# Kernel tuning notes

Measured on AMD Instinct MI355X. Metric: run time of the kernel, lower is better.

The kernel has to match this reference:

```python
import jax, jax.numpy as jnp
import numpy as np

INF_MIN = -10000.0
B, S, VOCAB = 256, 1024, 126
T = VOCAB + 2           # tag_size
START, END = T - 2, T - 1


def setup_inputs() -> dict:
    key = jax.random.key(0)
    k1, k2, k3 = jax.random.split(key, 3)
    features = jax.random.normal(k1, (B, S, T), dtype=jnp.float32)
    batch_len = jax.random.randint(k2, (B,), 1, S + 1, dtype=jnp.int32)
    transitions = jax.random.normal(k3, (T, T), dtype=jnp.float32)
    # CRF structural constraints set at init: nothing transitions INTO start,
    # nothing transitions OUT of end.
    transitions = transitions.at[:, START].set(INF_MIN).at[END, :].set(INF_MIN)
    return {"features": features, "batch_len": batch_len, "transitions": transitions}


def reference(features, batch_len, transitions):
    # features: [B, S, T], batch_len: [B], transitions: [T, T]
    b, s, t = features.shape
    alpha0 = jnp.full((b, t), INF_MIN, dtype=features.dtype).at[:, START].set(0.0)
    feats_t = jnp.transpose(features, (1, 0, 2))  # [S, B, T]

    def step(carry, feats):
        alpha, rem = carry
        # score[b, i, j] = emit[b, i] + trans[i, j] + alpha[b, j]
        scores = feats[:, :, None] + transitions[None, :, :] + alpha[:, None, :]
        alpha_next = jax.nn.logsumexp(scores, axis=2)  # [B, T]
        alive = (rem > 0)[:, None]
        alpha = jnp.where(alive, alpha_next, alpha)
        return (alpha, rem - 1), None

    (alpha, _), _ = jax.lax.scan(step, (alpha0, batch_len), feats_t)
    alpha = alpha + transitions[END][None, :]
    return jax.nn.logsumexp(alpha, axis=1)  # [B]
```

## Files before the change

### kernel.cpp

```cpp
#include <hip/hip_runtime.h>

#define BB 256
#define SS 1024
#define TT 128
#define ST 126
#define EN 127
#define IMIN -10000.0f
#define L2E 1.4426950408889634f
#define LN2f 0.6931471805599453f
#define QS 40

__global__ __launch_bounds__(512, 1) void crf_fwd(const float* __restrict__ feats,
                                                  const int* __restrict__ blen,
                                                  const float* __restrict__ trans,
                                                  float* __restrict__ out)
{
    const int tid = threadIdx.x;
    const int i   = tid >> 2;
    const int q   = tid & 3;
    const int b   = blockIdx.x;

    __shared__ __align__(16) float vbuf[2][4 * QS];
    __shared__ __align__(16) float featbuf[2][8 * TT];
    __shared__ __align__(16) float wout[TT];
    __shared__ __align__(16) float red[8];

    const float* fb = feats + (size_t)b * (SS * TT);
    const int L = blen[b];

    *(float2*)(&featbuf[0][tid * 2]) = *(const float2*)(fb + tid * 2);
    float f0 = fb[i];

    float4 P[8];
    {
        const float* trow = trans + i * TT + q * 32;
        #pragma unroll
        for (int k = 0; k < 8; ++k) {
            float4 tv = *(const float4*)(trow + 4 * k);
            P[k].x = tv.x * L2E; P[k].y = tv.y * L2E;
            P[k].z = tv.z * L2E; P[k].w = tv.w * L2E;
        }
    }
    float rm = -3.4e38f;
    #pragma unroll
    for (int k = 0; k < 8; ++k)
        rm = fmaxf(rm, fmaxf(fmaxf(P[k].x, P[k].y), fmaxf(P[k].z, P[k].w)));
    rm = fmaxf(rm, __shfl_xor(rm, 1));
    rm = fmaxf(rm, __shfl_xor(rm, 2));

    float S = 0.f;
    #pragma unroll
    for (int k = 0; k < 8; ++k) {
        P[k].x = exp2f(P[k].x - rm); P[k].y = exp2f(P[k].y - rm);
        P[k].z = exp2f(P[k].z - rm); P[k].w = exp2f(P[k].w - rm);
        S += (P[k].x + P[k].y) + (P[k].z + P[k].w);
    }
    S += __shfl_xor(S, 1);
    S += __shfl_xor(S, 2);

    float rmc = fmaxf(rm, 0.f);
    float A1 = fmaf(f0, L2E, (IMIN * L2E) + rmc +
                    log2f(fmaf(S, exp2f(rm - rmc), exp2f(-rmc))));

    if (tid == 0) red[0] = A1;
    __syncthreads();
    float sh = red[0];
    if (q == 0) vbuf[0][(i >> 5) * QS + (i & 31)] = exp2f(A1 - sh);
    __syncthreads();

    int cur = 0;
    float2 fnx = *(const float2*)(fb + 8 * TT + tid * 2);

    for (int ch = 0; ; ++ch) {
        if (8 * ch + 8 < L) {
            *(float2*)(&featbuf[(ch + 1) & 1][tid * 2]) = fnx;
            int cn = min(8 * ch + 16, SS - 8);
            fnx = *(const float2*)(fb + cn * TT + tid * 2);
        }
        const int sLo = (ch == 0) ? 1 : 8 * ch;
        const int sHi = min(8 * ch + 8, L);
        for (int s = sLo; s < sHi; ++s) {
            const float* vb = &vbuf[cur][q * QS];
            float v0f = vbuf[cur][0];
            float fv  = featbuf[ch & 1][((s & 7) << 7) + i];
            float dsh = log2f(v0f);
            float cf  = exp2f(fmaf(fv, L2E, rm - dsh));

            float a0 = 0.f, a1 = 0.f, a2 = 0.f, a3 = 0.f;
            #pragma unroll
            for (int k = 0; k < 8; ++k) {
                float4 vv = *(const float4*)(vb + 4 * k);
                a0 = fmaf(P[k].x, vv.x, a0);
                a1 = fmaf(P[k].y, vv.y, a1);
                a2 = fmaf(P[k].z, vv.z, a2);
                a3 = fmaf(P[k].w, vv.w, a3);
            }
            float part = (a0 + a1) + (a2 + a3);
            part += __shfl_xor(part, 1);
            part += __shfl_xor(part, 2);

            float vn = cf * part;
            sh += dsh;
            if (q == 0) vbuf[cur ^ 1][(i >> 5) * QS + (i & 31)] = vn;
            __syncthreads();
            cur ^= 1;
        }
        if (8 * ch + 8 >= L) break;
    }

    float vL = vbuf[cur][(i >> 5) * QS + (i & 31)];
    float w  = fmaf(trans[EN * TT + i], L2E, sh + log2f(vL));
    if (q == 0) wout[i] = w;
    __syncthreads();
    if (tid < 64) {
        float w0 = wout[tid], w1 = wout[tid + 64];
        float mm = fmaxf(w0, w1);
        #pragma unroll
        for (int off = 1; off < 64; off <<= 1) mm = fmaxf(mm, __shfl_xor(mm, off));
        float ss = exp2f(w0 - mm) + exp2f(w1 - mm);
        #pragma unroll
        for (int off = 1; off < 64; off <<= 1) ss += __shfl_xor(ss, off);
        if (tid == 0) out[b] = (mm + log2f(ss)) * LN2f;
    }
}

extern "C" void kernel_launch(void* const* d_in, const int* in_sizes, int n_in,
                              void* d_out, int out_size, void* d_ws, size_t ws_size,
                              hipStream_t stream) {
    const float* feats = (const float*)d_in[0];
    const int*   blen  = (const int*)d_in[1];
    const float* trans = (const float*)d_in[2];
    float*       o     = (float*)d_out;
    crf_fwd<<<dim3(BB), dim3(512), 0, stream>>>(feats, blen, trans, o);
}
```

Before: 372.3 us.

## Remap threads to 4-row x 16-column tiles with DPP row reductions

Each thread now holds 4 rows by 8 columns of the exponentiated transition matrix instead of 1 row by 32 columns. Per step it reads 8 shared-memory values instead of 32, reuses each value across 4 rows, and reduces across 16 lanes with DPP row_shr moves instead of shuffles. The state buffer gets a new padded layout, and the per-step barrier becomes an inline s_waitcnt plus s_barrier. The cost is a longer 16-lane reduction chain and four reductions per thread, with the select keeping only one row's result.

```diff
diff --git a/kernel.cpp b/kernel.cpp
--- a/kernel.cpp
+++ b/kernel.cpp
@@ -3,12 +3,23 @@
 #define BB 256
 #define SS 1024
 #define TT 128
-#define ST 126
 #define EN 127
 #define IMIN -10000.0f
 #define L2E 1.4426950408889634f
 #define LN2f 0.6931471805599453f
-#define QS 40
+
+template<int CTRL>
+__device__ __forceinline__ float dpp_mov(float x) {
+    return __int_as_float(__builtin_amdgcn_update_dpp(
+        0, __float_as_int(x), CTRL, 0xF, 0xF, true));
+}
+__device__ __forceinline__ float rowsum16(float x) {
+    x += dpp_mov<0x121>(x);
+    x += dpp_mov<0x122>(x);
+    x += dpp_mov<0x124>(x);
+    x += dpp_mov<0x128>(x);
+    return x;
+}
 
 __global__ __launch_bounds__(512, 1) void crf_fwd(const float* __restrict__ feats,
                                                   const int* __restrict__ blen,
@@ -16,11 +27,13 @@
                                                   float* __restrict__ out)
 {
     const int tid = threadIdx.x;
-    const int i   = tid >> 2;
-    const int q   = tid & 3;
+    const int c   = tid & 15;
+    const int g   = tid >> 4;
+    const int m3  = c & 3;
+    const int wrow = 4 * g + m3;
     const int b   = blockIdx.x;
 
-    __shared__ __align__(16) float vbuf[2][4 * QS];
+    __shared__ __align__(16) float vst[2][144];
     __shared__ __align__(16) float featbuf[2][8 * TT];
     __shared__ __align__(16) float wout[TT];
     __shared__ __align__(16) float red[8];
@@ -29,43 +42,64 @@
     const int L = blen[b];
 
     *(float2*)(&featbuf[0][tid * 2]) = *(const float2*)(fb + tid * 2);
-    float f0 = fb[i];
 
-    float4 P[8];
-    {
-        const float* trow = trans + i * TT + q * 32;
-        #pragma unroll
-        for (int k = 0; k < 8; ++k) {
-            float4 tv = *(const float4*)(trow + 4 * k);
-            P[k].x = tv.x * L2E; P[k].y = tv.y * L2E;
-            P[k].z = tv.z * L2E; P[k].w = tv.w * L2E;
-        }
+    const int voff = 8 * c + 4 * ((c >> 2) & 1);
+    const int widx = 8 * (wrow >> 3) + 4 * ((wrow >> 5) & 1) + (wrow & 7);
+
+    const float* tb = trans + (4 * g) * TT + 8 * c;
+    float4 P0L = *(const float4*)(tb);
+    float4 P0H = *(const float4*)(tb + 4);
+    float4 P1L = *(const float4*)(tb + TT);
+    float4 P1H = *(const float4*)(tb + TT + 4);
+    float4 P2L = *(const float4*)(tb + 2 * TT);
+    float4 P2H = *(const float4*)(tb + 2 * TT + 4);
+    float4 P3L = *(const float4*)(tb + 3 * TT);
+    float4 P3H = *(const float4*)(tb + 3 * TT + 4);
+#define SC4(Pv) Pv.x *= L2E; Pv.y *= L2E; Pv.z *= L2E; Pv.w *= L2E
+    SC4(P0L); SC4(P0H); SC4(P1L); SC4(P1H);
+    SC4(P2L); SC4(P2H); SC4(P3L); SC4(P3H);
+#undef SC4
+
+#define LMAX(Pl, Ph) fmaxf(fmaxf(fmaxf(Pl.x, Pl.y), fmaxf(Pl.z, Pl.w)), \
+                           fmaxf(fmaxf(Ph.x, Ph.y), fmaxf(Ph.z, Ph.w)))
+    float rm0 = LMAX(P0L, P0H), rm1 = LMAX(P1L, P1H);
+    float rm2 = LMAX(P2L, P2H), rm3 = LMAX(P3L, P3H);
+#undef LMAX
+    #pragma unroll
+    for (int off = 1; off < 16; off <<= 1) {
+        rm0 = fmaxf(rm0, __shfl_xor(rm0, off));
+        rm1 = fmaxf(rm1, __shfl_xor(rm1, off));
+        rm2 = fmaxf(rm2, __shfl_xor(rm2, off));
+        rm3 = fmaxf(rm3, __shfl_xor(rm3, off));
     }
-    float rm = -3.4e38f;
+#define NRM(Pv, r) Pv.x = exp2f(Pv.x - r); Pv.y = exp2f(Pv.y - r); \
+                   Pv.z = exp2f(Pv.z - r); Pv.w = exp2f(Pv.w - r)
+    NRM(P0L, rm0); NRM(P0H, rm0); NRM(P1L, rm1); NRM(P1H, rm1);
+    NRM(P2L, rm2); NRM(P2H, rm2); NRM(P3L, rm3); NRM(P3H, rm3);
+#undef NRM
+#define LSUM(Pl, Ph) (((Pl.x + Pl.y) + (Pl.z + Pl.w)) + \
+                      ((Ph.x + Ph.y) + (Ph.z + Ph.w)))
+    float S0 = LSUM(P0L, P0H), S1 = LSUM(P1L, P1H);
+    float S2 = LSUM(P2L, P2H), S3 = LSUM(P3L, P3H);
+#undef LSUM
     #pragma unroll
-    for (int k = 0; k < 8; ++k)
-        rm = fmaxf(rm, fmaxf(fmaxf(P[k].x, P[k].y), fmaxf(P[k].z, P[k].w)));
-    rm = fmaxf(rm, __shfl_xor(rm, 1));
-    rm = fmaxf(rm, __shfl_xor(rm, 2));
+    for (int off = 1; off < 16; off <<= 1) {
+        S0 += __shfl_xor(S0, off); S1 += __shfl_xor(S1, off);
+        S2 += __shfl_xor(S2, off); S3 += __shfl_xor(S3, off);
+    }
 
-    float S = 0.f;
-    #pragma unroll
-    for (int k = 0; k < 8; ++k) {
-        P[k].x = exp2f(P[k].x - rm); P[k].y = exp2f(P[k].y - rm);
-        P[k].z = exp2f(P[k].z - rm); P[k].w = exp2f(P[k].w - rm);
-        S += (P[k].x + P[k].y) + (P[k].z + P[k].w);
-    }
-    S += __shfl_xor(S, 1);
-    S += __shfl_xor(S, 2);
+    const float rmW = m3 == 0 ? rm0 : m3 == 1 ? rm1 : m3 == 2 ? rm2 : rm3;
+    const float SW  = m3 == 0 ? S0  : m3 == 1 ? S1  : m3 == 2 ? S2  : S3;
 
-    float rmc = fmaxf(rm, 0.f);
-    float A1 = fmaf(f0, L2E, (IMIN * L2E) + rmc +
-                    log2f(fmaf(S, exp2f(rm - rmc), exp2f(-rmc))));
+    float f0w = fb[wrow];
+    float rmc = fmaxf(rmW, 0.f);
+    float A1w = fmaf(f0w, L2E, (IMIN * L2E) + rmc +
+                     log2f(fmaf(SW, exp2f(rmW - rmc), exp2f(-rmc))));
 
-    if (tid == 0) red[0] = A1;
+    if (tid == 0) red[0] = A1w;
     __syncthreads();
     float sh = red[0];
-    if (q == 0) vbuf[0][(i >> 5) * QS + (i & 31)] = exp2f(A1 - sh);
+    if (c < 4) vst[0][widx] = exp2f(A1w - sh);
     __syncthreads();
 
     int cur = 0;
@@ -80,37 +114,56 @@
         const int sLo = (ch == 0) ? 1 : 8 * ch;
         const int sHi = min(8 * ch + 8, L);
         for (int s = sLo; s < sHi; ++s) {
-            const float* vb = &vbuf[cur][q * QS];
-            float v0f = vbuf[cur][0];
-            float fv  = featbuf[ch & 1][((s & 7) << 7) + i];
+            const float* vp = &vst[cur][voff];
+            float v0f = vst[cur][0];
+            float fv  = featbuf[ch & 1][((s & 7) << 7) + wrow];
+            float4 va  = *(const float4*)(vp);
+            float4 vb4 = *(const float4*)(vp + 4);
+
             float dsh = log2f(v0f);
-            float cf  = exp2f(fmaf(fv, L2E, rm - dsh));
+            float cf  = exp2f(fmaf(fv, L2E, rmW - dsh));
 
-            float a0 = 0.f, a1 = 0.f, a2 = 0.f, a3 = 0.f;
-            #pragma unroll
-            for (int k = 0; k < 8; ++k) {
-                float4 vv = *(const float4*)(vb + 4 * k);
-                a0 = fmaf(P[k].x, vv.x, a0);
-                a1 = fmaf(P[k].y, vv.y, a1);
-                a2 = fmaf(P[k].z, vv.z, a2);
-                a3 = fmaf(P[k].w, vv.w, a3);
-            }
-            float part = (a0 + a1) + (a2 + a3);
-            part += __shfl_xor(part, 1);
-            part += __shfl_xor(part, 2);
+            float p0 = P0L.x * va.x;
+            p0 = fmaf(P0L.y, va.y, p0);  p0 = fmaf(P0L.z, va.z, p0);
+            p0 = fmaf(P0L.w, va.w, p0);  p0 = fmaf(P0H.x, vb4.x, p0);
+            p0 = fmaf(P0H.y, vb4.y, p0); p0 = fmaf(P0H.z, vb4.z, p0);
+            p0 = fmaf(P0H.w, vb4.w, p0);
+            float p1 = P1L.x * va.x;
+            p1 = fmaf(P1L.y, va.y, p1);  p1 = fmaf(P1L.z, va.z, p1);
+            p1 = fmaf(P1L.w, va.w, p1);  p1 = fmaf(P1H.x, vb4.x, p1);
+            p1 = fmaf(P1H.y, vb4.y, p1); p1 = fmaf(P1H.z, vb4.z, p1);
+            p1 = fmaf(P1H.w, vb4.w, p1);
+            float p2 = P2L.x * va.x;
+            p2 = fmaf(P2L.y, va.y, p2);  p2 = fmaf(P2L.z, va.z, p2);
+            p2 = fmaf(P2L.w, va.w, p2);  p2 = fmaf(P2H.x, vb4.x, p2);
+            p2 = fmaf(P2H.y, vb4.y, p2); p2 = fmaf(P2H.z, vb4.z, p2);
+            p2 = fmaf(P2H.w, vb4.w, p2);
+            float p3 = P3L.x * va.x;
+            p3 = fmaf(P3L.y, va.y, p3);  p3 = fmaf(P3L.z, va.z, p3);
+            p3 = fmaf(P3L.w, va.w, p3);  p3 = fmaf(P3H.x, vb4.x, p3);
+            p3 = fmaf(P3H.y, vb4.y, p3); p3 = fmaf(P3H.z, vb4.z, p3);
+            p3 = fmaf(P3H.w, vb4.w, p3);
 
-            float vn = cf * part;
+            p0 = rowsum16(p0); p1 = rowsum16(p1);
+            p2 = rowsum16(p2); p3 = rowsum16(p3);
+
+            float totW = m3 == 0 ? p0 : m3 == 1 ? p1 : m3 == 2 ? p2 : p3;
+            float vn = cf * totW;
             sh += dsh;
-            if (q == 0) vbuf[cur ^ 1][(i >> 5) * QS + (i & 31)] = vn;
-            __syncthreads();
+            if (c < 4) vst[cur ^ 1][widx] = vn;
+            asm volatile("s_waitcnt lgkmcnt(0)\n\ts_barrier" ::: "memory");
             cur ^= 1;
         }
         if (8 * ch + 8 >= L) break;
     }
 
-    float vL = vbuf[cur][(i >> 5) * QS + (i & 31)];
-    float w  = fmaf(trans[EN * TT + i], L2E, sh + log2f(vL));
-    if (q == 0) wout[i] = w;
+    __syncthreads();
+    if (tid < TT) {
+        int j = tid;
+        int ridx = 8 * (j >> 3) + 4 * ((j >> 5) & 1) + (j & 7);
+        float vL = vst[cur][ridx];
+        wout[j] = fmaf(trans[EN * TT + j], L2E, sh + log2f(vL));
+    }
     __syncthreads();
     if (tid < 64) {
         float w0 = wout[tid], w1 = wout[tid + 64];
```

Result: slower. 381.6 us (+2.5%).

## Halve block size: 4 rows per 8-lane group with DPP reductions and raw barrier

Applied to the files above, without the earlier changes.

Each thread now computes 4 output tags over a 16-column slice instead of 1 tag over 32 columns, so the block drops from 512 to 256 threads (4 waves). Cross-lane sums use DPP moves instead of shuffles, and the per-step __syncthreads is replaced by an inline waitcnt+s_barrier. The goal is a shorter serial step: fewer waves at each barrier, cheaper reductions, and vectorized shared loads and stores. In exchange each thread holds 64 transition weights in registers and does more serial work per step.

```diff
diff --git a/kernel.cpp b/kernel.cpp
--- a/kernel.cpp
+++ b/kernel.cpp
@@ -3,24 +3,41 @@
 #define BB 256
 #define SS 1024
 #define TT 128
-#define ST 126
 #define EN 127
 #define IMIN -10000.0f
 #define L2E 1.4426950408889634f
 #define LN2f 0.6931471805599453f
-#define QS 40
+#define CS 20
 
-__global__ __launch_bounds__(512, 1) void crf_fwd(const float* __restrict__ feats,
+template<int CTRL>
+__device__ __forceinline__ float dpp_mov(float x) {
+    return __int_as_float(__builtin_amdgcn_update_dpp(
+        0, __float_as_int(x), CTRL, 0xF, 0xF, true));
+}
+__device__ __forceinline__ float sum8(float x) {
+    x += dpp_mov<0xB1>(x);
+    x += dpp_mov<0x4E>(x);
+    x += dpp_mov<0x141>(x);
+    return x;
+}
+__device__ __forceinline__ float max8(float x) {
+    x = fmaxf(x, dpp_mov<0xB1>(x));
+    x = fmaxf(x, dpp_mov<0x4E>(x));
+    x = fmaxf(x, dpp_mov<0x141>(x));
+    return x;
+}
+
+__global__ __launch_bounds__(256, 1) void crf_fwd(const float* __restrict__ feats,
                                                   const int* __restrict__ blen,
                                                   const float* __restrict__ trans,
                                                   float* __restrict__ out)
 {
     const int tid = threadIdx.x;
-    const int i   = tid >> 2;
-    const int q   = tid & 3;
+    const int c   = tid & 7;
+    const int g   = tid >> 3;
     const int b   = blockIdx.x;
 
-    __shared__ __align__(16) float vbuf[2][4 * QS];
+    __shared__ __align__(16) float vst[2][8 * CS];
     __shared__ __align__(16) float featbuf[2][8 * TT];
     __shared__ __align__(16) float wout[TT];
     __shared__ __align__(16) float red[8];
@@ -28,89 +45,115 @@
     const float* fb = feats + (size_t)b * (SS * TT);
     const int L = blen[b];
 
-    *(float2*)(&featbuf[0][tid * 2]) = *(const float2*)(fb + tid * 2);
-    float f0 = fb[i];
+    *(float4*)(&featbuf[0][tid * 4]) = *(const float4*)(fb + tid * 4);
 
-    float4 P[8];
+    float4 P[4][4];
     {
-        const float* trow = trans + i * TT + q * 32;
+        const float* tb = trans + (4 * g) * TT + 16 * c;
         #pragma unroll
-        for (int k = 0; k < 8; ++k) {
-            float4 tv = *(const float4*)(trow + 4 * k);
-            P[k].x = tv.x * L2E; P[k].y = tv.y * L2E;
-            P[k].z = tv.z * L2E; P[k].w = tv.w * L2E;
+        for (int m = 0; m < 4; ++m)
+            #pragma unroll
+            for (int k = 0; k < 4; ++k) {
+                float4 t = *(const float4*)(tb + m * TT + 4 * k);
+                t.x *= L2E; t.y *= L2E; t.z *= L2E; t.w *= L2E;
+                P[m][k] = t;
+            }
+    }
+    float rm[4], S[4];
+    #pragma unroll
+    for (int m = 0; m < 4; ++m) {
+        float r = -3.4e38f;
+        #pragma unroll
+        for (int k = 0; k < 4; ++k)
+            r = fmaxf(r, fmaxf(fmaxf(P[m][k].x, P[m][k].y),
+                               fmaxf(P[m][k].z, P[m][k].w)));
+        rm[m] = max8(r);
+        float s = 0.f;
+        #pragma unroll
+        for (int k = 0; k < 4; ++k) {
+            P[m][k].x = exp2f(P[m][k].x - rm[m]);
+            P[m][k].y = exp2f(P[m][k].y - rm[m]);
+            P[m][k].z = exp2f(P[m][k].z - rm[m]);
+            P[m][k].w = exp2f(P[m][k].w - rm[m]);
+            s += (P[m][k].x + P[m][k].y) + (P[m][k].z + P[m][k].w);
         }
+        S[m] = sum8(s);
     }
-    float rm = -3.4e38f;
+
+    float4 f0v = *(const float4*)(fb + 4 * g);
+    float f0a[4] = {f0v.x, f0v.y, f0v.z, f0v.w};
+    float A1[4];
     #pragma unroll
-    for (int k = 0; k < 8; ++k)
-        rm = fmaxf(rm, fmaxf(fmaxf(P[k].x, P[k].y), fmaxf(P[k].z, P[k].w)));
-    rm = fmaxf(rm, __shfl_xor(rm, 1));
-    rm = fmaxf(rm, __shfl_xor(rm, 2));
+    for (int m = 0; m < 4; ++m) {
+        float rmc = fmaxf(rm[m], 0.f);
+        A1[m] = fmaf(f0a[m], L2E, (IMIN * L2E) + rmc +
+                     log2f(fmaf(S[m], exp2f(rm[m] - rmc), exp2f(-rmc))));
+    }
 
-    float S = 0.f;
-    #pragma unroll
-    for (int k = 0; k < 8; ++k) {
-        P[k].x = exp2f(P[k].x - rm); P[k].y = exp2f(P[k].y - rm);
-        P[k].z = exp2f(P[k].z - rm); P[k].w = exp2f(P[k].w - rm);
-        S += (P[k].x + P[k].y) + (P[k].z + P[k].w);
-    }
-    S += __shfl_xor(S, 1);
-    S += __shfl_xor(S, 2);
-
-    float rmc = fmaxf(rm, 0.f);
-    float A1 = fmaf(f0, L2E, (IMIN * L2E) + rmc +
-                    log2f(fmaf(S, exp2f(rm - rmc), exp2f(-rmc))));
-
-    if (tid == 0) red[0] = A1;
+    if (tid == 0) red[0] = A1[0];
     __syncthreads();
     float sh = red[0];
-    if (q == 0) vbuf[0][(i >> 5) * QS + (i & 31)] = exp2f(A1 - sh);
+    if (c == 0) {
+        float4 v0w = make_float4(exp2f(A1[0] - sh), exp2f(A1[1] - sh),
+                                 exp2f(A1[2] - sh), exp2f(A1[3] - sh));
+        *(float4*)(&vst[0][CS * (g >> 2) + 4 * (g & 3)]) = v0w;
+    }
     __syncthreads();
 
     int cur = 0;
-    float2 fnx = *(const float2*)(fb + 8 * TT + tid * 2);
+    float4 fnx = *(const float4*)(fb + 8 * TT + tid * 4);
 
     for (int ch = 0; ; ++ch) {
         if (8 * ch + 8 < L) {
-            *(float2*)(&featbuf[(ch + 1) & 1][tid * 2]) = fnx;
+            *(float4*)(&featbuf[(ch + 1) & 1][tid * 4]) = fnx;
             int cn = min(8 * ch + 16, SS - 8);
-            fnx = *(const float2*)(fb + cn * TT + tid * 2);
+            fnx = *(const float4*)(fb + cn * TT + tid * 4);
         }
         const int sLo = (ch == 0) ? 1 : 8 * ch;
         const int sHi = min(8 * ch + 8, L);
         for (int s = sLo; s < sHi; ++s) {
-            const float* vb = &vbuf[cur][q * QS];
-            float v0f = vbuf[cur][0];
-            float fv  = featbuf[ch & 1][((s & 7) << 7) + i];
+            const float* vp = &vst[cur][CS * c];
+            float  v0f = vst[cur][0];
+            float4 ff  = *(const float4*)(&featbuf[ch & 1][((s & 7) << 7) + 4 * g]);
+            float4 v0  = *(const float4*)(vp);
+            float4 v1  = *(const float4*)(vp + 4);
+            float4 v2  = *(const float4*)(vp + 8);
+            float4 v3  = *(const float4*)(vp + 12);
+
             float dsh = log2f(v0f);
-            float cf  = exp2f(fmaf(fv, L2E, rm - dsh));
+            float ffa[4] = {ff.x, ff.y, ff.z, ff.w};
 
-            float a0 = 0.f, a1 = 0.f, a2 = 0.f, a3 = 0.f;
+            float vnv[4];
             #pragma unroll
-            for (int k = 0; k < 8; ++k) {
-                float4 vv = *(const float4*)(vb + 4 * k);
-                a0 = fmaf(P[k].x, vv.x, a0);
-                a1 = fmaf(P[k].y, vv.y, a1);
-                a2 = fmaf(P[k].z, vv.z, a2);
-                a3 = fmaf(P[k].w, vv.w, a3);
+            for (int m = 0; m < 4; ++m) {
+                float a0 = P[m][0].x * v0.x, a1 = P[m][0].y * v0.y;
+                float a2 = P[m][0].z * v0.z, a3 = P[m][0].w * v0.w;
+                a0 = fmaf(P[m][1].x, v1.x, a0); a1 = fmaf(P[m][1].y, v1.y, a1);
+                a2 = fmaf(P[m][1].z, v1.z, a2); a3 = fmaf(P[m][1].w, v1.w, a3);
+                a0 = fmaf(P[m][2].x, v2.x, a0); a1 = fmaf(P[m][2].y, v2.y, a1);
+                a2 = fmaf(P[m][2].z, v2.z, a2); a3 = fmaf(P[m][2].w, v2.w, a3);
+                a0 = fmaf(P[m][3].x, v3.x, a0); a1 = fmaf(P[m][3].y, v3.y, a1);
+                a2 = fmaf(P[m][3].z, v3.z, a2); a3 = fmaf(P[m][3].w, v3.w, a3);
+                float t = sum8(((a0 + a1) + (a2 + a3)));
+                float cf = exp2f(fmaf(ffa[m], L2E, rm[m] - dsh));
+                vnv[m] = cf * t;
             }
-            float part = (a0 + a1) + (a2 + a3);
-            part += __shfl_xor(part, 1);
-            part += __shfl_xor(part, 2);
-
-            float vn = cf * part;
             sh += dsh;
-            if (q == 0) vbuf[cur ^ 1][(i >> 5) * QS + (i & 31)] = vn;
-            __syncthreads();
+            if (c == 0)
+                *(float4*)(&vst[cur ^ 1][CS * (g >> 2) + 4 * (g & 3)]) =
+                    make_float4(vnv[0], vnv[1], vnv[2], vnv[3]);
+            asm volatile("s_waitcnt lgkmcnt(0)\n\ts_barrier" ::: "memory");
             cur ^= 1;
         }
         if (8 * ch + 8 >= L) break;
     }
 
-    float vL = vbuf[cur][(i >> 5) * QS + (i & 31)];
-    float w  = fmaf(trans[EN * TT + i], L2E, sh + log2f(vL));
-    if (q == 0) wout[i] = w;
+    __syncthreads();
+    if (tid < TT) {
+        int j = tid;
+        float vL = vst[cur][CS * (j >> 4) + (j & 15)];
+        wout[j] = fmaf(trans[EN * TT + j], L2E, sh + log2f(vL));
+    }
     __syncthreads();
     if (tid < 64) {
         float w0 = wout[tid], w1 = wout[tid + 64];
@@ -131,5 +174,5 @@
     const int*   blen  = (const int*)d_in[1];
     const float* trans = (const float*)d_in[2];
     float*       o     = (float*)d_out;
-    crf_fwd<<<dim3(BB), dim3(512), 0, stream>>>(feats, blen, trans, o);
+    crf_fwd<<<dim3(BB), dim3(256), 0, stream>>>(feats, blen, trans, o);
 }
```

Result: slower. 408.4 us (+9.7%).

## Remap CRF recurrence to 8 lanes per 2 rows with DPP reductions

Applied to the files above, without the earlier changes.

Changes the thread mapping from 4 lanes per tag row to 8 lanes per pair of rows, so each lane holds two rows of 16 transition weights. Cross-lane reductions move from shuffles to DPP row operations. The per-step normaliser is taken with readfirstlane plus a hardware reciprocal instead of log2 and exp2. The step barrier becomes a raw s_waitcnt plus s_barrier. The aim is to shorten the serial per-timestep critical path, at the cost of a padded shared-state layout and approximate rcp precision.

```diff
diff --git a/kernel.cpp b/kernel.cpp
--- a/kernel.cpp
+++ b/kernel.cpp
@@ -3,12 +3,29 @@
 #define BB 256
 #define SS 1024
 #define TT 128
-#define ST 126
 #define EN 127
 #define IMIN -10000.0f
 #define L2E 1.4426950408889634f
 #define LN2f 0.6931471805599453f
-#define QS 40
+#define CS 20
+
+template<int CTRL>
+__device__ __forceinline__ float dpp_mov(float x) {
+    return __int_as_float(__builtin_amdgcn_update_dpp(
+        0, __float_as_int(x), CTRL, 0xF, 0xF, true));
+}
+__device__ __forceinline__ float sum8(float x) {
+    x += dpp_mov<0xB1>(x);
+    x += dpp_mov<0x4E>(x);
+    x += dpp_mov<0x141>(x);
+    return x;
+}
+__device__ __forceinline__ float max8(float x) {
+    x = fmaxf(x, dpp_mov<0xB1>(x));
+    x = fmaxf(x, dpp_mov<0x4E>(x));
+    x = fmaxf(x, dpp_mov<0x141>(x));
+    return x;
+}
 
 __global__ __launch_bounds__(512, 1) void crf_fwd(const float* __restrict__ feats,
                                                   const int* __restrict__ blen,
@@ -16,11 +33,11 @@
                                                   float* __restrict__ out)
 {
     const int tid = threadIdx.x;
-    const int i   = tid >> 2;
-    const int q   = tid & 3;
+    const int c   = tid & 7;
+    const int rp  = tid >> 3;
     const int b   = blockIdx.x;
 
-    __shared__ __align__(16) float vbuf[2][4 * QS];
+    __shared__ __align__(16) float vst[2][8 * CS];
     __shared__ __align__(16) float featbuf[2][8 * TT];
     __shared__ __align__(16) float wout[TT];
     __shared__ __align__(16) float red[8];
@@ -29,43 +46,49 @@
     const int L = blen[b];
 
     *(float2*)(&featbuf[0][tid * 2]) = *(const float2*)(fb + tid * 2);
-    float f0 = fb[i];
 
-    float4 P[8];
-    {
-        const float* trow = trans + i * TT + q * 32;
-        #pragma unroll
-        for (int k = 0; k < 8; ++k) {
-            float4 tv = *(const float4*)(trow + 4 * k);
-            P[k].x = tv.x * L2E; P[k].y = tv.y * L2E;
-            P[k].z = tv.z * L2E; P[k].w = tv.w * L2E;
-        }
-    }
-    float rm = -3.4e38f;
-    #pragma unroll
-    for (int k = 0; k < 8; ++k)
-        rm = fmaxf(rm, fmaxf(fmaxf(P[k].x, P[k].y), fmaxf(P[k].z, P[k].w)));
-    rm = fmaxf(rm, __shfl_xor(rm, 1));
-    rm = fmaxf(rm, __shfl_xor(rm, 2));
+    const float* tb = trans + (2 * rp) * TT + 16 * c;
+    float4 Pa0 = *(const float4*)(tb);
+    float4 Pa1 = *(const float4*)(tb + 4);
+    float4 Pa2 = *(const float4*)(tb + 8);
+    float4 Pa3 = *(const float4*)(tb + 12);
+    float4 Pb0 = *(const float4*)(tb + TT);
+    float4 Pb1 = *(const float4*)(tb + TT + 4);
+    float4 Pb2 = *(const float4*)(tb + TT + 8);
+    float4 Pb3 = *(const float4*)(tb + TT + 12);
+#define SC4(Pv) Pv.x *= L2E; Pv.y *= L2E; Pv.z *= L2E; Pv.w *= L2E
+    SC4(Pa0); SC4(Pa1); SC4(Pa2); SC4(Pa3);
+    SC4(Pb0); SC4(Pb1); SC4(Pb2); SC4(Pb3);
+#undef SC4
+#define LMAX4(Pv) fmaxf(fmaxf(Pv.x, Pv.y), fmaxf(Pv.z, Pv.w))
+    float rm0 = max8(fmaxf(fmaxf(LMAX4(Pa0), LMAX4(Pa1)),
+                           fmaxf(LMAX4(Pa2), LMAX4(Pa3))));
+    float rm1 = max8(fmaxf(fmaxf(LMAX4(Pb0), LMAX4(Pb1)),
+                           fmaxf(LMAX4(Pb2), LMAX4(Pb3))));
+#undef LMAX4
+#define NRM4(Pv, r) Pv.x = exp2f(Pv.x - r); Pv.y = exp2f(Pv.y - r); \
+                    Pv.z = exp2f(Pv.z - r); Pv.w = exp2f(Pv.w - r)
+    NRM4(Pa0, rm0); NRM4(Pa1, rm0); NRM4(Pa2, rm0); NRM4(Pa3, rm0);
+    NRM4(Pb0, rm1); NRM4(Pb1, rm1); NRM4(Pb2, rm1); NRM4(Pb3, rm1);
+#undef NRM4
+#define SUM4(Pv) ((Pv.x + Pv.y) + (Pv.z + Pv.w))
+    float S0 = sum8((SUM4(Pa0) + SUM4(Pa1)) + (SUM4(Pa2) + SUM4(Pa3)));
+    float S1 = sum8((SUM4(Pb0) + SUM4(Pb1)) + (SUM4(Pb2) + SUM4(Pb3)));
+#undef SUM4
 
-    float S = 0.f;
-    #pragma unroll
-    for (int k = 0; k < 8; ++k) {
-        P[k].x = exp2f(P[k].x - rm); P[k].y = exp2f(P[k].y - rm);
-        P[k].z = exp2f(P[k].z - rm); P[k].w = exp2f(P[k].w - rm);
-        S += (P[k].x + P[k].y) + (P[k].z + P[k].w);
-    }
-    S += __shfl_xor(S, 1);
-    S += __shfl_xor(S, 2);
+    float2 f0v = *(const float2*)(fb + 2 * rp);
+    float rmc0 = fmaxf(rm0, 0.f), rmc1 = fmaxf(rm1, 0.f);
+    float A1a = fmaf(f0v.x, L2E, (IMIN * L2E) + rmc0 +
+                     log2f(fmaf(S0, exp2f(rm0 - rmc0), exp2f(-rmc0))));
+    float A1b = fmaf(f0v.y, L2E, (IMIN * L2E) + rmc1 +
+                     log2f(fmaf(S1, exp2f(rm1 - rmc1), exp2f(-rmc1))));
 
-    float rmc = fmaxf(rm, 0.f);
-    float A1 = fmaf(f0, L2E, (IMIN * L2E) + rmc +
-                    log2f(fmaf(S, exp2f(rm - rmc), exp2f(-rmc))));
-
-    if (tid == 0) red[0] = A1;
+    if (tid == 0) red[0] = A1a;
     __syncthreads();
     float sh = red[0];
-    if (q == 0) vbuf[0][(i >> 5) * QS + (i & 31)] = exp2f(A1 - sh);
+    if (c == 0)
+        *(float2*)(&vst[0][CS * (rp >> 3) + 2 * (rp & 7)]) =
+            make_float2(exp2f(A1a - sh), exp2f(A1b - sh));
     __syncthreads();
 
     int cur = 0;
@@ -80,37 +103,56 @@
         const int sLo = (ch == 0) ? 1 : 8 * ch;
         const int sHi = min(8 * ch + 8, L);
         for (int s = sLo; s < sHi; ++s) {
-            const float* vb = &vbuf[cur][q * QS];
-            float v0f = vbuf[cur][0];
-            float fv  = featbuf[ch & 1][((s & 7) << 7) + i];
-            float dsh = log2f(v0f);
-            float cf  = exp2f(fmaf(fv, L2E, rm - dsh));
+            const float* vp = &vst[cur][CS * c];
+            float4 v0 = *(const float4*)(vp);
+            float4 v1 = *(const float4*)(vp + 4);
+            float4 v2 = *(const float4*)(vp + 8);
+            float4 v3 = *(const float4*)(vp + 12);
+            float2 ffv = *(const float2*)(&featbuf[ch & 1][((s & 7) << 7) + 2 * rp]);
 
-            float a0 = 0.f, a1 = 0.f, a2 = 0.f, a3 = 0.f;
-            #pragma unroll
-            for (int k = 0; k < 8; ++k) {
-                float4 vv = *(const float4*)(vb + 4 * k);
-                a0 = fmaf(P[k].x, vv.x, a0);
-                a1 = fmaf(P[k].y, vv.y, a1);
-                a2 = fmaf(P[k].z, vv.z, a2);
-                a3 = fmaf(P[k].w, vv.w, a3);
-            }
-            float part = (a0 + a1) + (a2 + a3);
-            part += __shfl_xor(part, 1);
-            part += __shfl_xor(part, 2);
+            float v0u = __int_as_float(
+                __builtin_amdgcn_readfirstlane(__float_as_int(v0.x)));
+            float rv0 = __builtin_amdgcn_rcpf(v0u);
+            float efa = exp2f(fmaf(ffv.x, L2E, rm0)) * rv0;
+            float efb = exp2f(fmaf(ffv.y, L2E, rm1)) * rv0;
 
-            float vn = cf * part;
-            sh += dsh;
-            if (q == 0) vbuf[cur ^ 1][(i >> 5) * QS + (i & 31)] = vn;
-            __syncthreads();
+            float a0 = Pa0.x * v0.x, a1 = Pa0.y * v0.y;
+            float a2 = Pa0.z * v0.z, a3 = Pa0.w * v0.w;
+            a0 = fmaf(Pa1.x, v1.x, a0); a1 = fmaf(Pa1.y, v1.y, a1);
+            a2 = fmaf(Pa1.z, v1.z, a2); a3 = fmaf(Pa1.w, v1.w, a3);
+            a0 = fmaf(Pa2.x, v2.x, a0); a1 = fmaf(Pa2.y, v2.y, a1);
+            a2 = fmaf(Pa2.z, v2.z, a2); a3 = fmaf(Pa2.w, v2.w, a3);
+            a0 = fmaf(Pa3.x, v3.x, a0); a1 = fmaf(Pa3.y, v3.y, a1);
+            a2 = fmaf(Pa3.z, v3.z, a2); a3 = fmaf(Pa3.w, v3.w, a3);
+            float pa = sum8((a0 + a1) + (a2 + a3));
+
+            float b0 = Pb0.x * v0.x, b1 = Pb0.y * v0.y;
+            float b2 = Pb0.z * v0.z, b3 = Pb0.w * v0.w;
+            b0 = fmaf(Pb1.x, v1.x, b0); b1 = fmaf(Pb1.y, v1.y, b1);
+            b2 = fmaf(Pb1.z, v1.z, b2); b3 = fmaf(Pb1.w, v1.w, b3);
+            b0 = fmaf(Pb2.x, v2.x, b0); b1 = fmaf(Pb2.y, v2.y, b1);
+            b2 = fmaf(Pb2.z, v2.z, b2); b3 = fmaf(Pb2.w, v2.w, b3);
+            b0 = fmaf(Pb3.x, v3.x, b0); b1 = fmaf(Pb3.y, v3.y, b1);
+            b2 = fmaf(Pb3.z, v3.z, b2); b3 = fmaf(Pb3.w, v3.w, b3);
+            float pb = sum8((b0 + b1) + (b2 + b3));
+
+            float vna = efa * pa, vnb = efb * pb;
+            sh += log2f(v0u);
+            if (c == 0)
+                *(float2*)(&vst[cur ^ 1][CS * (rp >> 3) + 2 * (rp & 7)]) =
+                    make_float2(vna, vnb);
+            asm volatile("s_waitcnt lgkmcnt(0)\n\ts_barrier" ::: "memory");
             cur ^= 1;
         }
         if (8 * ch + 8 >= L) break;
     }
 
-    float vL = vbuf[cur][(i >> 5) * QS + (i & 31)];
-    float w  = fmaf(trans[EN * TT + i], L2E, sh + log2f(vL));
-    if (q == 0) wout[i] = w;
+    __syncthreads();
+    if (tid < TT) {
+        int j = tid;
+        float vL = vst[cur][CS * (j >> 4) + (j & 15)];
+        wout[j] = fmaf(trans[EN * TT + j], L2E, sh + log2f(vL));
+    }
     __syncthreads();
     if (tid < 64) {
         float w0 = wout[tid], w1 = wout[tid + 64];
```

New measurement: 389.0 us. 4.5% more time.
